# Performance work log

Measured on AMD Instinct MI355X. Metric: run time of the kernel, lower is better.

Reference implementation:

```python
import jax, jax.numpy as jnp
import numpy as np

NEG = -1e30  # finite stand-in for -inf (keeps gradients NaN-free)
BLANK = 0    # PyTorch nn.CTCLoss default blank index


def setup_inputs() -> dict:
    key = jax.random.key(0)
    k1, k2, k3 = jax.random.split(key, 3)
    T, B, C, S = 512, 1024, 63, 25
    # model emits log-probabilities (log_softmax output), as nn.CTCLoss expects
    log_probs = jax.nn.log_softmax(jax.random.normal(k1, (T, B, C), jnp.float32), axis=-1)
    targets = jax.random.randint(k2, (B, S), 1, C, dtype=jnp.int32)        # labels in [1, C)
    target_lengths = jax.random.randint(k3, (B,), 10, S + 1, dtype=jnp.int32)
    return {"log_probs": log_probs, "targets": targets, "target_lengths": target_lengths}


def _ctc_loss(log_probs, targets, target_lengths):
    # log_probs: [T, B, C]; targets: [B, S] padded; target_lengths: [B]
    T, B, C = log_probs.shape
    S = targets.shape[1]
    L = 2 * S + 1  # extended target: blank-interleaved

    ext = jnp.zeros((B, L), targets.dtype).at[:, 1::2].set(targets)  # [B, L]
    prev2 = jnp.concatenate([jnp.full((B, 2), -1, ext.dtype), ext[:, :-2]], axis=1)
    skip = (ext != BLANK) & (ext != prev2)  # allow alpha[s-2] transition

    # t = 0 init: only positions 0 (blank) and 1 (first label) reachable
    lp0 = log_probs[0]  # [B, C]
    alpha0 = jnp.full((B, L), NEG, log_probs.dtype)
    alpha0 = alpha0.at[:, 0].set(lp0[:, BLANK])
    alpha0 = alpha0.at[:, 1].set(jnp.take_along_axis(lp0, ext[:, 1:2], axis=1)[:, 0])

    def step(alpha, lp_t):  # alpha: [B, L], lp_t: [B, C]
        lp_ext = jnp.take_along_axis(lp_t, ext, axis=1)  # [B, L]
        a1 = alpha
        a2 = jnp.pad(alpha[:, :-1], ((0, 0), (1, 0)), constant_values=NEG)
        a3 = jnp.where(skip, jnp.pad(alpha[:, :-2], ((0, 0), (2, 0)), constant_values=NEG), NEG)
        m = jnp.maximum(jnp.maximum(a1, a2), a3)
        new = m + jnp.log(jnp.exp(a1 - m) + jnp.exp(a2 - m) + jnp.exp(a3 - m)) + lp_ext
        return new, None

    alpha_T, _ = jax.lax.scan(step, alpha0, log_probs[1:])

    # log-likelihood = logaddexp of the last two reachable positions (2*len, 2*len-1)
    idx = jnp.stack([2 * target_lengths - 1, 2 * target_lengths], axis=1)  # [B, 2]
    a_fin = jnp.take_along_axis(alpha_T, idx, axis=1)
    ll = jnp.logaddexp(a_fin[:, 0], a_fin[:, 1])
    nll = -ll
    nll = jnp.where(nll > 0.5e30, 0.0, nll)  # zero_infinity=True
    # PyTorch reduction='mean': divide each loss by its target length, then batch mean
    return jnp.mean(nll / jnp.maximum(target_lengths, 1).astype(nll.dtype))


def reference(log_probs, targets, target_lengths):
    return _ctc_loss(log_probs, targets, target_lengths)
```

## Files before the change

kernel.cpp:

```cpp
#include <hip/hip_runtime.h>


#define TT 512
#define BB 1024
#define CC 63
#define SS 25
#define DP 24
#define NEGV (-1e30f)
#define LN2F 0.69314718055994531f

__device__ __forceinline__ float shr1f(float x, float fill) {
  return __int_as_float(__builtin_amdgcn_update_dpp(
      __float_as_int(fill), __float_as_int(x), 0x138, 0xF, 0xF, false));
}
__device__ __forceinline__ int shr1i(int x, int fill) {
  return __builtin_amdgcn_update_dpp(fill, x, 0x138, 0xF, 0xF, false);
}
__device__ __forceinline__ float shl1f(float x, float fill) {
  return __int_as_float(__builtin_amdgcn_update_dpp(
      __float_as_int(fill), __float_as_int(x), 0x130, 0xF, 0xF, false));
}
__device__ __forceinline__ int shl1i(int x, int fill) {
  return __builtin_amdgcn_update_dpp(fill, x, 0x130, 0xF, 0xF, false);
}
__device__ __forceinline__ int iclamp126(int d) {
  return d < -126 ? -126 : (d > 126 ? 126 : d);
}

__global__ __launch_bounds__(256) void ctc_fb_kernel(
    const float* __restrict__ logp,
    const int* __restrict__ targets,
    const int* __restrict__ tlen,
    float* __restrict__ loss) {
  const int lane = threadIdx.x & 63;
  const int wid = threadIdx.x >> 6;
  const int b = (blockIdx.x << 2) + wid;
  const int* tg = targets + b * SS;
  const int len = tlen[b];

  int e = 0;
  float skf = 0.0f;
  float skf2 = 0.0f;
  if (lane & 1) {
    const int i = lane >> 1;
    if (i < SS) {
      e = tg[i];
      skf = (i == 0 || e != tg[i - 1]) ? 1.0f : 0.0f;
      if (i + 1 < SS) skf2 = (tg[i + 1] != tg[i]) ? 1.0f : 0.0f;
    }
  }

  const unsigned SB = (unsigned)(BB * CC) * 4u;
  const char* base = (const char*)logp;
  const unsigned off0 = (unsigned)(b * CC + e) * 4u;
#define LDR(O) (*(const float*)(base + (O)))

  float Af = (lane <= 1) ? __expf(LDR(off0)) : 0.0f;
  int M2f = 0;
  float F1f = 1.0f, F2f = skf;
  float Ab = (lane == 2 * len - 1 || lane == 2 * len) ? 1.0f : 0.0f;
  int M2b = 0;
  float F1b = 1.0f, F2b = skf2;

  float pfF[DP], pfB[DP];
  unsigned offF = off0 + SB;
  unsigned offB = off0 + 511u * SB;
#pragma unroll
  for (int j = 0; j < DP; ++j) {
    pfF[j] = LDR(offF); offF += SB;
    pfB[j] = LDR(offB); offB -= SB;
  }

#define RENF() {                                               \
    int e2 = (int)(__float_as_uint(Af) >> 23) - 127;           \
    Af = ldexpf(Af, -e2);                                      \
    int m2n = M2f + e2;                                        \
    int m2a = shr1i(m2n, 0);                                   \
    M2f = (Af == 0.0f) ? m2a : m2n;                            \
    int s1 = shr1i(M2f, 0), s2 = shr1i(s1, 0);                 \
    F1f = ldexpf(1.0f, iclamp126(s1 - M2f));                   \
    F2f = skf * ldexpf(1.0f, iclamp126(s2 - M2f));             \
  }
#define RENB() {                                               \
    int e2 = (int)(__float_as_uint(Ab) >> 23) - 127;           \
    Ab = ldexpf(Ab, -e2);                                      \
    int m2n = M2b + e2;                                        \
    int m2a = shl1i(m2n, 0);                                   \
    M2b = (Ab == 0.0f) ? m2a : m2n;                            \
    int s1 = shl1i(M2b, 0), s2 = shl1i(s1, 0);                 \
    F1b = ldexpf(1.0f, iclamp126(s1 - M2b));                   \
    F2b = skf2 * ldexpf(1.0f, iclamp126(s2 - M2b));            \
  }
#define STEPF(J, PFLAG) {                                      \
    const float P = __expf(pfF[(J)]);                          \
    const float c1 = P * F1f, c2 = P * F2f;                    \
    const float x1 = shr1f(Af, 0.0f);                          \
    const float pa = P * Af;                                   \
    const float x2 = shr1f(x1, 0.0f);                          \
    Af = fmaf(c2, x2, fmaf(c1, x1, pa));                       \
    if (PFLAG) { pfF[(J)] = LDR(offF); offF += SB; }           \
  }
#define STEPB(J, PFLAG) {                                      \
    const float P = __expf(pfB[(J)]);                          \
    const float P1 = shl1f(P, 0.0f);                           \
    const float P2 = shl1f(P1, 0.0f);                          \
    const float c1 = F1b * P1, c2 = F2b * P2;                  \
    const float y1 = shl1f(Ab, 0.0f);                          \
    const float pb = P * Ab;                                   \
    const float y2 = shl1f(y1, 0.0f);                          \
    Ab = fmaf(c2, y2, fmaf(c1, y1, pb));                       \
    if (PFLAG) { pfB[(J)] = LDR(offB); offB -= SB; }           \
  }

  STEPB(0, true)

  for (int blk = 0; blk < 9; ++blk) {
#pragma unroll
    for (int j = 0; j < DP; ++j) {
      STEPF(j, true)
      STEPB((j + 1) % DP, true)
      if (j == 11 || j == 23) { RENF() RENB() }
    }
  }
#pragma unroll
  for (int j = 0; j < DP; ++j) {
    STEPF(j, j <= 14)
    STEPB((j + 1) % DP, j <= 14)
    if (j == 11 || j == 23) { RENF() RENB() }
  }
#pragma unroll
  for (int j = 0; j < 15; ++j) {
    STEPF(j, false)
    STEPB(j + 1, false)
    if (j == 11) { RENF() RENB() }
  }

  const float laf = fmaxf((float)M2f * LN2F + logf(Af), NEGV);
  const float lab = fmaxf((float)M2b * LN2F + logf(Ab), NEGV);
  float v = (lane <= 50) ? laf + lab : -2e30f;
  float m = v;
#pragma unroll
  for (int o = 32; o; o >>= 1) m = fmaxf(m, __shfl_xor(m, o));
  float s = __expf(v - m);
#pragma unroll
  for (int o = 32; o; o >>= 1) s += __shfl_xor(s, o);
  if (lane == 0) {
    const float ll = m + logf(s);
    float nll = -ll;
    if (!(nll <= 0.5e30f)) nll = 0.0f;
    const int dl = len > 1 ? len : 1;
    loss[b] = nll / (float)dl;
  }
}

__global__ __launch_bounds__(256) void ctc_reduce_kernel(
    const float* __restrict__ loss, float* __restrict__ out) {
  float s = 0.f;
  for (int i = threadIdx.x; i < BB; i += 256) s += loss[i];
#pragma unroll
  for (int off = 32; off; off >>= 1) s += __shfl_down(s, off);
  __shared__ float sm[4];
  if ((threadIdx.x & 63) == 0) sm[threadIdx.x >> 6] = s;
  __syncthreads();
  if (threadIdx.x == 0) out[0] = (sm[0] + sm[1] + sm[2] + sm[3]) / (float)BB;
}

extern "C" void kernel_launch(void* const* d_in, const int* in_sizes, int n_in,
                              void* d_out, int out_size, void* d_ws, size_t ws_size,
                              hipStream_t stream) {
  const float* logp  = (const float*)d_in[0];
  const int* targets = (const int*)d_in[1];
  const int* tlen    = (const int*)d_in[2];
  float* out  = (float*)d_out;
  float* loss = (float*)d_ws;
  hipLaunchKernelGGL(ctc_fb_kernel, dim3(BB / 4), dim3(256), 0, stream,
                     logp, targets, tlen, loss);
  hipLaunchKernelGGL(ctc_reduce_kernel, dim3(1), dim3(256), 0, stream, loss, out);
}
```

Before: 31.96 us.

## Fuse final batch reduction into main kernel via fixed-point atomics and ticket

Removes the separate reduction kernel launch. Each wave atomically adds its per-sample loss, scaled to 64-bit fixed point, into a workspace accumulator, and the last wave to take a ticket writes the mean. A memset zeroes the workspace before the launch. The prefetch depth also goes from 24 to 28, with the loop trip counts and renormalization points adjusted to match. Fixed-point accumulation stays deterministic but truncates precision, and it assumes per-sample losses are non-negative.

Result: slower. 59.60 us (+86.5%).

```diff
diff --git a/kernel.cpp b/kernel.cpp
--- a/kernel.cpp
+++ b/kernel.cpp
@@ -5,9 +5,10 @@
 #define BB 1024
 #define CC 63
 #define SS 25
-#define DP 24
+#define DP 28
 #define NEGV (-1e30f)
 #define LN2F 0.69314718055994531f
+#define SCALE 8589934592.0
 
 __device__ __forceinline__ float shr1f(float x, float fill) {
   return __int_as_float(__builtin_amdgcn_update_dpp(
@@ -31,7 +32,9 @@
     const float* __restrict__ logp,
     const int* __restrict__ targets,
     const int* __restrict__ tlen,
-    float* __restrict__ loss) {
+    unsigned long long* __restrict__ wsum,
+    unsigned int* __restrict__ wticket,
+    float* __restrict__ out) {
   const int lane = threadIdx.x & 63;
   const int wid = threadIdx.x >> 6;
   const int b = (blockIdx.x << 2) + wid;
@@ -114,25 +117,24 @@
 
   STEPB(0, true)
 
-  for (int blk = 0; blk < 9; ++blk) {
+  for (int blk = 0; blk < 8; ++blk) {
 #pragma unroll
     for (int j = 0; j < DP; ++j) {
       STEPF(j, true)
       STEPB((j + 1) % DP, true)
-      if (j == 11 || j == 23) { RENF() RENB() }
+      if (j == 9 || j == 19 || j == 27) { RENF() RENB() }
     }
   }
 #pragma unroll
   for (int j = 0; j < DP; ++j) {
-    STEPF(j, j <= 14)
-    STEPB((j + 1) % DP, j <= 14)
-    if (j == 11 || j == 23) { RENF() RENB() }
+    STEPF(j, j <= 2)
+    STEPB((j + 1) % DP, j <= 2)
+    if (j == 9 || j == 19 || j == 27) { RENF() RENB() }
   }
 #pragma unroll
-  for (int j = 0; j < 15; ++j) {
+  for (int j = 0; j < 3; ++j) {
     STEPF(j, false)
     STEPB(j + 1, false)
-    if (j == 11) { RENF() RENB() }
   }
 
   const float laf = fmaxf((float)M2f * LN2F + logf(Af), NEGV);
@@ -144,25 +146,23 @@
   float s = __expf(v - m);
 #pragma unroll
   for (int o = 32; o; o >>= 1) s += __shfl_xor(s, o);
+
   if (lane == 0) {
     const float ll = m + logf(s);
     float nll = -ll;
     if (!(nll <= 0.5e30f)) nll = 0.0f;
     const int dl = len > 1 ? len : 1;
-    loss[b] = nll / (float)dl;
+    const float smp = nll / (float)dl;
+    const unsigned long long q = (unsigned long long)((double)smp * SCALE);
+    atomicAdd(wsum, q);
+    __threadfence();
+    const unsigned t = atomicAdd(wticket, 1u);
+    if (t == (unsigned)(BB - 1)) {
+      __threadfence();
+      const unsigned long long tot = atomicAdd(wsum, 0ull);
+      out[0] = (float)(((double)tot / SCALE) / (double)BB);
+    }
   }
-}
-
-__global__ __launch_bounds__(256) void ctc_reduce_kernel(
-    const float* __restrict__ loss, float* __restrict__ out) {
-  float s = 0.f;
-  for (int i = threadIdx.x; i < BB; i += 256) s += loss[i];
-#pragma unroll
-  for (int off = 32; off; off >>= 1) s += __shfl_down(s, off);
-  __shared__ float sm[4];
-  if ((threadIdx.x & 63) == 0) sm[threadIdx.x >> 6] = s;
-  __syncthreads();
-  if (threadIdx.x == 0) out[0] = (sm[0] + sm[1] + sm[2] + sm[3]) / (float)BB;
 }
 
 extern "C" void kernel_launch(void* const* d_in, const int* in_sizes, int n_in,
@@ -171,9 +171,10 @@
   const float* logp  = (const float*)d_in[0];
   const int* targets = (const int*)d_in[1];
   const int* tlen    = (const int*)d_in[2];
-  float* out  = (float*)d_out;
-  float* loss = (float*)d_ws;
+  hipMemsetAsync(d_ws, 0, 16, stream);
   hipLaunchKernelGGL(ctc_fb_kernel, dim3(BB / 4), dim3(256), 0, stream,
-                     logp, targets, tlen, loss);
-  hipLaunchKernelGGL(ctc_reduce_kernel, dim3(1), dim3(256), 0, stream, loss, out);
+                     logp, targets, tlen,
+                     (unsigned long long*)d_ws,
+                     (unsigned int*)((char*)d_ws + 8),
+                     (float*)d_out);
 }
```
